# Kernel tuning notes

Measured on AMD Instinct MI355X. Metric: run time of the kernel, lower is better.

The kernel has to match this reference:

```python
import jax, jax.numpy as jnp
import numpy as np

DIM, D_STATE, D_CONV, EXPAND = 512, 16, 4, 2
D_INNER = EXPAND * DIM            # 1024
DT_RANK = (DIM + 15) // 16        # 32
B, L = 2, 2048


def setup_inputs() -> dict:
    key = jax.random.key(0)
    ks = jax.random.split(key, 12)
    s_in = 1.0 / np.sqrt(DIM)
    s_xp = 1.0 / np.sqrt(D_INNER)
    s_dt = 1.0 / np.sqrt(DT_RANK)
    return {
        "x": jax.random.normal(ks[0], (B, L, DIM), jnp.float32),
        "ln_g": jnp.ones((DIM,), jnp.float32),
        "ln_b": jnp.zeros((DIM,), jnp.float32),
        "W_in": jax.random.normal(ks[1], (2 * D_INNER, DIM), jnp.float32) * s_in,
        "conv_w": jax.random.normal(ks[2], (D_INNER, D_CONV), jnp.float32) * 0.5,
        "conv_b": jax.random.normal(ks[3], (D_INNER,), jnp.float32) * 0.1,
        "W_xproj": jax.random.normal(ks[4], (DT_RANK + 2 * D_STATE, D_INNER), jnp.float32) * s_xp,
        "W_dt": jax.random.normal(ks[5], (D_INNER, DT_RANK), jnp.float32) * s_dt,
        "b_dt": jax.random.normal(ks[6], (D_INNER,), jnp.float32) * 0.1 - 4.0,  # softplus -> small dt
        "A_log": jnp.log(jax.random.uniform(ks[7], (D_INNER, D_STATE), jnp.float32, 1.0, 16.0)),
        "Dp": jax.random.normal(ks[8], (D_INNER,), jnp.float32),
        "W_out": jax.random.normal(ks[9], (DIM, D_INNER), jnp.float32) * s_xp,
    }


def _layernorm(x, g, b, eps=1e-5):
    mu = jnp.mean(x, -1, keepdims=True)
    var = jnp.mean(jnp.square(x - mu), -1, keepdims=True)
    return (x - mu) * jax.lax.rsqrt(var + eps) * g + b


def reference(x, ln_g, ln_b, W_in, conv_w, conv_b, W_xproj, W_dt, b_dt, A_log, Dp, W_out):
    h = _layernorm(x, ln_g, ln_b)
    # input projection -> [B,L,2*d_inner]
    xz = jnp.einsum('bld,ed->ble', h, W_in)
    xp, z = jnp.split(xz, 2, axis=-1)
    # depthwise causal conv1d over time (kernel d_conv), then SiLU
    xp_pad = jnp.pad(xp, ((0, 0), (D_CONV - 1, 0), (0, 0)))
    xc = conv_b
    for k in range(D_CONV):
        xc = xc + xp_pad[:, k:k + L, :] * conv_w[:, k]
    xc = jax.nn.silu(xc)
    # x_proj -> dt, B, C
    proj = jnp.einsum('bld,ed->ble', xc, W_xproj)
    dt_r = proj[..., :DT_RANK]
    Bm = proj[..., DT_RANK:DT_RANK + D_STATE]          # [B,L,n]
    Cm = proj[..., DT_RANK + D_STATE:]                 # [B,L,n]
    dt = jax.nn.softplus(jnp.einsum('blr,dr->bld', dt_r, W_dt) + b_dt)  # [B,L,d]
    A = -jnp.exp(A_log)                                # [d,n]
    dA = jnp.exp(jnp.einsum('bld,dn->bldn', dt, A))    # [B,L,d,n]
    dBx = dt[..., None] * Bm[:, :, None, :] * xc[..., None]  # [B,L,d,n]
    # selective scan over time (time-major for lax.scan)
    def step(s, inp):
        dA_t, dBx_t, C_t = inp
        s = s * dA_t + dBx_t                           # [B,d,n]
        y_t = jnp.einsum('bdn,bn->bd', s, C_t)
        return s, y_t
    s0 = jnp.zeros((B, D_INNER, D_STATE), xc.dtype)
    _, ys = jax.lax.scan(step, s0,
                         (jnp.moveaxis(dA, 1, 0), jnp.moveaxis(dBx, 1, 0), jnp.moveaxis(Cm, 1, 0)))
    y = jnp.moveaxis(ys, 0, 1)                         # [B,L,d]
    y = y + xc * Dp
    y = y * jax.nn.silu(z)
    out = jnp.einsum('bld,ed->ble', y, W_out)
    return x + out  # dropout is identity in eval mode
```

## Files before the change

### kernel.cpp

```cpp
#include <hip/hip_runtime.h>
#include <hip/hip_bf16.h>
#include <math.h>

#define B_      2
#define L_      2048
#define DIM_    512
#define DINNER  1024
#define DTRANK  32
#define DSTATE  16
#define DCONV   4
#define BL      (B_ * L_)
#define NCHUNK  64
#define CLEN    (L_ / NCHUNK)

typedef __attribute__((ext_vector_type(8))) short bf16x8;
typedef __attribute__((ext_vector_type(4))) float f32x4;

static __device__ __forceinline__ unsigned short f2bf(float f) {
  __hip_bfloat16 h = __float2bfloat16(f);
  return *(unsigned short*)&h;
}
static __device__ __forceinline__ float bf2f(unsigned short u) {
  return __uint_as_float(((unsigned int)u) << 16);
}

static __device__ __forceinline__ void gload16(const void* g, void* l) {
  __builtin_amdgcn_global_load_lds(
      (const __attribute__((address_space(1))) void*)g,
      (__attribute__((address_space(3))) void*)l, 16, 0, 0);
}

static __device__ __forceinline__ float softplus_f(float acc) {
  return (acc > 20.f) ? acc : __logf(1.f + __expf(acc));
}

__global__ __launch_bounds__(256) void cvt_ln_kernel(
    const float* __restrict__ s0, const float* __restrict__ s1,
    const float* __restrict__ s2, __hip_bfloat16* __restrict__ d0,
    __hip_bfloat16* __restrict__ d1, __hip_bfloat16* __restrict__ d2,
    const float* __restrict__ x, const float* __restrict__ g,
    const float* __restrict__ b, __hip_bfloat16* __restrict__ h) {
  int blk = blockIdx.x;
  if (blk < 1600) {
    int i = (blk * 256 + threadIdx.x) * 4;
    const float* s; __hip_bfloat16* d; int off;
    if (i < 1048576)            { s = s0; d = d0; off = i; }
    else if (i < 1048576+65536) { s = s1; d = d1; off = i - 1048576; }
    else                        { s = s2; d = d2; off = i - 1114112; }
    float4 v = *(const float4*)(s + off);
    d[off + 0] = __float2bfloat16(v.x);
    d[off + 1] = __float2bfloat16(v.y);
    d[off + 2] = __float2bfloat16(v.z);
    d[off + 3] = __float2bfloat16(v.w);
    return;
  }
  int row = (blk - 1600) * 4 + (threadIdx.x >> 6);
  int lane = threadIdx.x & 63;
  const float* xr = x + (size_t)row * DIM_;
  float v[8];
  float sum = 0.f;
#pragma unroll
  for (int i = 0; i < 8; i++) { v[i] = xr[lane + i * 64]; sum += v[i]; }
#pragma unroll
  for (int o = 32; o > 0; o >>= 1) sum += __shfl_xor(sum, o, 64);
  float mu = sum * (1.f / DIM_);
  float vs = 0.f;
#pragma unroll
  for (int i = 0; i < 8; i++) { float dd = v[i] - mu; vs += dd * dd; }
#pragma unroll
  for (int o = 32; o > 0; o >>= 1) vs += __shfl_xor(vs, o, 64);
  float rstd = rsqrtf(vs * (1.f / DIM_) + 1e-5f);
  __hip_bfloat16* hr = h + (size_t)row * DIM_;
#pragma unroll
  for (int i = 0; i < 8; i++) {
    int c = lane + i * 64;
    hr[c] = __float2bfloat16((v[i] - mu) * rstd * g[c] + b[c]);
  }
}

template <bool ADD_RES, bool OUT_BF16>
__global__ __launch_bounds__(256) void gemm_mfma_128(
    const __hip_bfloat16* __restrict__ A, int lda,
    const __hip_bfloat16* __restrict__ Bw, int ldb,
    const float* __restrict__ Res, int ldr,
    void* __restrict__ C, int ldc, int K) {
  __shared__ short As[128 * 64];
  __shared__ short Bs[128 * 64];
  int t = threadIdx.x;
  int n0 = blockIdx.x * 128, m0 = blockIdx.y * 128;
  int w = t >> 6, lane = t & 63;
  int wm = (w >> 1) * 64, wn = (w & 1) * 64;
  int l15 = lane & 15, quad = lane >> 4;
  int lr = lane >> 3, lc = (lane & 7) * 8;
  const short* Ag = (const short*)A + (size_t)(m0 + w * 32 + lr) * lda + lc;
  const short* Bg = (const short*)Bw + (size_t)(n0 + w * 32 + lr) * ldb + lc;
  f32x4 acc[4][4];
#pragma unroll
  for (int i = 0; i < 4; i++)
#pragma unroll
    for (int j = 0; j < 4; j++) acc[i][j] = (f32x4){0.f, 0.f, 0.f, 0.f};
  for (int k0 = 0; k0 < K; k0 += 64) {
    __syncthreads();
#pragma unroll
    for (int p = 0; p < 4; p++) {
      gload16(Ag + (size_t)(p * 8) * lda + k0, &As[(w * 32 + p * 8) * 64]);
      gload16(Bg + (size_t)(p * 8) * ldb + k0, &Bs[(w * 32 + p * 8) * 64]);
    }
    __syncthreads();
#pragma unroll
    for (int kk = 0; kk < 64; kk += 32) {
      bf16x8 af[4], bfr[4];
#pragma unroll
      for (int i = 0; i < 4; i++) {
        af[i] = *(const bf16x8*)&As[(wm + i * 16 + l15) * 64 + kk + quad * 8];
        bfr[i] = *(const bf16x8*)&Bs[(wn + i * 16 + l15) * 64 + kk + quad * 8];
      }
#pragma unroll
      for (int i = 0; i < 4; i++)
#pragma unroll
        for (int j = 0; j < 4; j++)
          acc[i][j] = __builtin_amdgcn_mfma_f32_16x16x32_bf16(
              af[i], bfr[j], acc[i][j], 0, 0, 0);
    }
  }
#pragma unroll
  for (int i = 0; i < 4; i++)
#pragma unroll
    for (int r = 0; r < 4; r++) {
      int row = m0 + wm + i * 16 + quad * 4 + r;
#pragma unroll
      for (int j = 0; j < 4; j++) {
        int col = n0 + wn + j * 16 + l15;
        float v = acc[i][j][r];
        if (ADD_RES) v += Res[(size_t)row * ldr + col];
        if (OUT_BF16)
          ((unsigned short*)C)[(size_t)row * ldc + col] = f2bf(v);
        else
          ((float*)C)[(size_t)row * ldc + col] = v;
      }
    }
}

template <bool ADD_RES>
__global__ __launch_bounds__(256) void gemm_mfma_64(
    const __hip_bfloat16* __restrict__ A, int lda,
    const __hip_bfloat16* __restrict__ Bw, int ldb,
    const float* __restrict__ Res, int ldr,
    float* __restrict__ C, int ldc, int K, size_t czs) {
  __shared__ short As[64 * 64];
  __shared__ short Bs[64 * 64];
  int t = threadIdx.x;
  int n0 = blockIdx.x * 64, m0 = blockIdx.y * 64;
  size_t kbase = (size_t)blockIdx.z * K;
  int w = t >> 6, lane = t & 63;
  int wm = (w >> 1) * 32, wn = (w & 1) * 32;
  int l15 = lane & 15, quad = lane >> 4;
  int lr = lane >> 3, lc = (lane & 7) * 8;
  const short* Ag = (const short*)A + (size_t)(m0 + w * 16 + lr) * lda + lc + kbase;
  const short* Bg = (const short*)Bw + (size_t)(n0 + w * 16 + lr) * ldb + lc + kbase;
  f32x4 acc[2][2];
#pragma unroll
  for (int i = 0; i < 2; i++)
#pragma unroll
    for (int j = 0; j < 2; j++) acc[i][j] = (f32x4){0.f, 0.f, 0.f, 0.f};
  for (int k0 = 0; k0 < K; k0 += 64) {
    __syncthreads();
#pragma unroll
    for (int p = 0; p < 2; p++) {
      gload16(Ag + (size_t)(p * 8) * lda + k0, &As[(w * 16 + p * 8) * 64]);
      gload16(Bg + (size_t)(p * 8) * ldb + k0, &Bs[(w * 16 + p * 8) * 64]);
    }
    __syncthreads();
#pragma unroll
    for (int kk = 0; kk < 64; kk += 32) {
      bf16x8 af[2], bfr[2];
#pragma unroll
      for (int i = 0; i < 2; i++) {
        af[i] = *(const bf16x8*)&As[(wm + i * 16 + l15) * 64 + kk + quad * 8];
        bfr[i] = *(const bf16x8*)&Bs[(wn + i * 16 + l15) * 64 + kk + quad * 8];
      }
#pragma unroll
      for (int i = 0; i < 2; i++)
#pragma unroll
        for (int j = 0; j < 2; j++)
          acc[i][j] = __builtin_amdgcn_mfma_f32_16x16x32_bf16(
              af[i], bfr[j], acc[i][j], 0, 0, 0);
    }
  }
  float* Cz = C + czs * blockIdx.z;
#pragma unroll
  for (int i = 0; i < 2; i++)
#pragma unroll
    for (int r = 0; r < 4; r++) {
      int row = m0 + wm + i * 16 + quad * 4 + r;
#pragma unroll
      for (int j = 0; j < 2; j++) {
        int col = n0 + wn + j * 16 + l15;
        float v = acc[i][j][r];
        if (ADD_RES) v += Res[(size_t)row * ldr + col];
        Cz[(size_t)row * ldc + col] = v;
      }
    }
}

__global__ __launch_bounds__(256) void gemm_proj_conv(
    const unsigned short* __restrict__ xzb,
    const __hip_bfloat16* __restrict__ Bw,
    const float* __restrict__ cw, const float* __restrict__ cb,
    __hip_bfloat16* __restrict__ xc_bf,
    float* __restrict__ C, size_t czs) {
  __shared__ short As[64 * 64];
  __shared__ short Bs[64 * 64];
  __shared__ float cws[256 * 4];
  __shared__ float cbs[256];
  int t = threadIdx.x;
  int m0 = blockIdx.y * 64;
  int kbase = blockIdx.z * 256;
  int w = t >> 6, lane = t & 63;
  int wm = (w >> 1) * 32, wn = (w & 1) * 32;
  int l15 = lane & 15, quad = lane >> 4;
  int lrB = lane >> 3, lcB = (lane & 7) * 8;
  const short* Bg = (const short*)Bw + (size_t)(w * 16 + lrB) * DINNER + lcB + kbase;
  *(float4*)&cws[t * 4] = *(const float4*)(cw + (size_t)(kbase + t) * 4);
  cbs[t] = cb[kbase + t];
  int ar = t >> 2, aq = t & 3;
  int bl = m0 + ar;
  int l = bl & (L_ - 1);
  f32x4 acc[2][2];
#pragma unroll
  for (int i = 0; i < 2; i++)
#pragma unroll
    for (int j = 0; j < 2; j++) acc[i][j] = (f32x4){0.f, 0.f, 0.f, 0.f};
  for (int k0 = 0; k0 < 256; k0 += 64) {
    __syncthreads();
#pragma unroll
    for (int p = 0; p < 2; p++)
      gload16(Bg + k0 + (size_t)(p * 8) * DINNER, &Bs[(w * 16 + p * 8) * 64]);
    int dl0 = k0 + aq * 16;
    const unsigned short* xrow = xzb + (size_t)bl * 2048 + kbase + dl0;
    float o[16];
#pragma unroll
    for (int cc = 0; cc < 16; cc++) o[cc] = cbs[dl0 + cc];
#pragma unroll
    for (int k = 0; k < 4; k++) {
      int off = 3 - k;
      bool ok = (l >= off);
      const unsigned short* src = xrow - (size_t)(ok ? off : 0) * 2048;
      bf16x8 v0 = *(const bf16x8*)(src);
      bf16x8 v1 = *(const bf16x8*)(src + 8);
#pragma unroll
      for (int cc = 0; cc < 8; cc++) {
        float xa = ok ? bf2f((unsigned short)v0[cc]) : 0.f;
        float xb = ok ? bf2f((unsigned short)v1[cc]) : 0.f;
        o[cc]     = fmaf(xa, cws[(dl0 + cc) * 4 + k], o[cc]);
        o[cc + 8] = fmaf(xb, cws[(dl0 + cc + 8) * 4 + k], o[cc + 8]);
      }
    }
    bf16x8 pa, pb;
#pragma unroll
    for (int cc = 0; cc < 8; cc++) {
      float va = o[cc] / (1.f + __expf(-o[cc]));
      float vb = o[cc + 8] / (1.f + __expf(-o[cc + 8]));
      pa[cc] = (short)f2bf(va);
      pb[cc] = (short)f2bf(vb);
    }
    *(bf16x8*)&As[ar * 64 + aq * 16] = pa;
    *(bf16x8*)&As[ar * 64 + aq * 16 + 8] = pb;
    unsigned short* xcd = (unsigned short*)xc_bf + (size_t)bl * DINNER + kbase + dl0;
    *(bf16x8*)xcd = pa;
    *(bf16x8*)(xcd + 8) = pb;
    __syncthreads();
#pragma unroll
    for (int kk = 0; kk < 64; kk += 32) {
      bf16x8 af[2], bfr[2];
#pragma unroll
      for (int i = 0; i < 2; i++) {
        af[i] = *(const bf16x8*)&As[(wm + i * 16 + l15) * 64 + kk + quad * 8];
        bfr[i] = *(const bf16x8*)&Bs[(wn + i * 16 + l15) * 64 + kk + quad * 8];
      }
#pragma unroll
      for (int i = 0; i < 2; i++)
#pragma unroll
        for (int j = 0; j < 2; j++)
          acc[i][j] = __builtin_amdgcn_mfma_f32_16x16x32_bf16(
              af[i], bfr[j], acc[i][j], 0, 0, 0);
    }
  }
  float* Cz = C + czs * blockIdx.z;
#pragma unroll
  for (int i = 0; i < 2; i++)
#pragma unroll
    for (int r = 0; r < 4; r++) {
      int row = m0 + wm + i * 16 + quad * 4 + r;
#pragma unroll
      for (int j = 0; j < 2; j++) {
        int col = wn + j * 16 + l15;
        Cz[(size_t)row * 64 + col] = acc[i][j][r];
      }
    }
}

__global__ __launch_bounds__(256) void dt_kernel(
    const float* __restrict__ pp, float* __restrict__ proj,
    const float* __restrict__ Wdt, const float* __restrict__ bdt,
    float* __restrict__ dt) {
  int blk = blockIdx.x;
  int dgrp = blk & 3;
  int bl0 = (blk >> 2) * 8;
  int tid = threadIdx.x;
  int d = dgrp * 256 + tid;
  __shared__ float pr[8 * 64];
  float w[32];
#pragma unroll
  for (int q = 0; q < 8; q++) {
    float4 wv = *(const float4*)(Wdt + (size_t)d * 32 + q * 4);
    w[q * 4 + 0] = wv.x; w[q * 4 + 1] = wv.y;
    w[q * 4 + 2] = wv.z; w[q * 4 + 3] = wv.w;
  }
  float bias = bdt[d];
  if (tid < 128) {
    int o4 = bl0 * 16 + tid;
    float4 v0 = ((const float4*)pp)[o4];
    float4 v1 = ((const float4*)pp)[o4 + 65536];
    float4 v2 = ((const float4*)pp)[o4 + 131072];
    float4 v3 = ((const float4*)pp)[o4 + 196608];
    float4 s;
    s.x = (v0.x + v1.x) + (v2.x + v3.x);
    s.y = (v0.y + v1.y) + (v2.y + v3.y);
    s.z = (v0.z + v1.z) + (v2.z + v3.z);
    s.w = (v0.w + v1.w) + (v2.w + v3.w);
    ((float4*)pr)[tid] = s;
    if (dgrp == 0) *(float4*)(proj + (size_t)bl0 * 64 + tid * 4) = s;
  }
  __syncthreads();
#pragma unroll
  for (int row = 0; row < 8; row++) {
    float a0 = 0.f, a1 = 0.f, a2 = 0.f, a3 = 0.f;
#pragma unroll
    for (int q = 0; q < 8; q++) {
      float4 pv = *(const float4*)&pr[row * 64 + q * 4];
      a0 = fmaf(pv.x, w[q * 4 + 0], a0);
      a1 = fmaf(pv.y, w[q * 4 + 1], a1);
      a2 = fmaf(pv.z, w[q * 4 + 2], a2);
      a3 = fmaf(pv.w, w[q * 4 + 3], a3);
    }
    float acc = bias + ((a0 + a1) + (a2 + a3));
    dt[(size_t)(bl0 + row) * DINNER + d] = softplus_f(acc);
  }
}

__global__ __launch_bounds__(256) void scan1_kernel(
    const float* __restrict__ dt, const __hip_bfloat16* __restrict__ xc_bf,
    const float* __restrict__ proj, const float* __restrict__ A_log,
    float* __restrict__ T, float* __restrict__ E) {
  int bid = blockIdx.x;
  int dgrp4 = bid & 15;
  int c = (bid >> 4) & (NCHUNK - 1);
  int b = bid >> 10;
  int tid = threadIdx.x;
  int dl = tid >> 2;
  int n4 = tid & 3;
  int d0 = dgrp4 * 64;
  int d = d0 + dl;
  int l0 = c * CLEN;
  __shared__ float dts[CLEN * 64];
  __shared__ float xcs[CLEN * 64];
  __shared__ float Bsh[CLEN * 16];
  for (int i = tid; i < CLEN * 16; i += 256) {
    int row = i >> 4, c4 = i & 15;
    *(float4*)&dts[row * 64 + c4 * 4] =
        *(const float4*)(dt + (size_t)(b * L_ + l0 + row) * DINNER + d0 + c4 * 4);
  }
  {
    int row = tid >> 3, c8 = tid & 7;
    bf16x8 v = *(const bf16x8*)((const unsigned short*)xc_bf +
                                (size_t)(b * L_ + l0 + row) * DINNER + d0 + c8 * 8);
#pragma unroll
    for (int k = 0; k < 8; k++)
      xcs[row * 64 + c8 * 8 + k] = bf2f((unsigned short)v[k]);
  }
  if (tid < CLEN * 4) {
    int row = tid >> 2, c4 = tid & 3;
    *(float4*)&Bsh[row * 16 + c4 * 4] =
        *(const float4*)(proj + (size_t)(b * L_ + l0 + row) * 64 + 32 + c4 * 4);
  }
  float4 av = *(const float4*)(A_log + (size_t)d * 16 + n4 * 4);
  float Aa[4] = {-__expf(av.x), -__expf(av.y), -__expf(av.z), -__expf(av.w)};
  __syncthreads();
  float Tn[4] = {1.f, 1.f, 1.f, 1.f};
  float En[4] = {0.f, 0.f, 0.f, 0.f};
#pragma unroll 8
  for (int l = 0; l < CLEN; l++) {
    float dtv = dts[l * 64 + dl];
    float dx = dtv * xcs[l * 64 + dl];
#pragma unroll
    for (int j = 0; j < 4; j++) {
      float dA = __expf(dtv * Aa[j]);
      Tn[j] *= dA;
      En[j] = En[j] * dA + dx * Bsh[l * 16 + n4 * 4 + j];
    }
  }
  size_t o = (((size_t)b * NCHUNK + c) * DINNER + d) * 16 + n4 * 4;
  *(float4*)&T[o] = *(float4*)Tn;
  *(float4*)&E[o] = *(float4*)En;
}

__global__ __launch_bounds__(256) void combine_kernel(
    float* __restrict__ T, const float* __restrict__ E) {
  int idx = blockIdx.x * 256 + threadIdx.x;
  int b = idx >> 14;
  int dn = idx & 16383;
  size_t base = (size_t)b * NCHUNK * (DINNER * 16) + dn;
  float s = 0.f;
#pragma unroll
  for (int batch = 0; batch < 4; batch++) {
    float t[16], e[16];
#pragma unroll
    for (int j = 0; j < 16; j++) {
      size_t o = base + (size_t)(batch * 16 + j) * (DINNER * 16);
      t[j] = T[o]; e[j] = E[o];
    }
#pragma unroll
    for (int j = 0; j < 16; j++) {
      T[base + (size_t)(batch * 16 + j) * (DINNER * 16)] = s;
      s = t[j] * s + e[j];
    }
  }
}

__global__ __launch_bounds__(256) void scan2_kernel(
    const float* __restrict__ dt, const __hip_bfloat16* __restrict__ xc_bf,
    const float* __restrict__ proj, const float* __restrict__ A_log,
    const float* __restrict__ Sstart, const float* __restrict__ Dp,
    unsigned short* __restrict__ xzb) {
  int bid = blockIdx.x;
  int dgrp = bid & 3;
  int c = (bid >> 2) & (NCHUNK - 1);
  int b = bid >> 8;
  int tid = threadIdx.x;
  int d = dgrp * 256 + tid;
  int l0 = c * CLEN;
  __shared__ float Bsh[CLEN * 16];
  __shared__ float Csh[CLEN * 16];
  for (int i = tid; i < CLEN * 16; i += 256) {
    int row = i >> 4, nn = i & 15;
    const float* pr = proj + (size_t)(b * L_ + l0 + row) * 64;
    Bsh[i] = pr[32 + nn];
    Csh[i] = pr[48 + nn];
  }
  float dtr[CLEN], xvr[CLEN];
  unsigned short zr[CLEN];
#pragma unroll
  for (int l = 0; l < CLEN; l++) {
    size_t bl = (size_t)(b * L_ + l0 + l);
    dtr[l] = dt[bl * DINNER + d];
    xvr[l] = __bfloat162float(xc_bf[bl * DINNER + d]);
    zr[l] = xzb[bl * 2048 + 1024 + d];
  }
  float Aa[16], s[16];
  size_t sb = (((size_t)b * NCHUNK + c) * DINNER + d) * 16;
#pragma unroll
  for (int q = 0; q < 4; q++) {
    float4 av = *(const float4*)(A_log + (size_t)d * 16 + q * 4);
    Aa[q * 4 + 0] = -__expf(av.x); Aa[q * 4 + 1] = -__expf(av.y);
    Aa[q * 4 + 2] = -__expf(av.z); Aa[q * 4 + 3] = -__expf(av.w);
    float4 sv = *(const float4*)(Sstart + sb + q * 4);
    s[q * 4 + 0] = sv.x; s[q * 4 + 1] = sv.y;
    s[q * 4 + 2] = sv.z; s[q * 4 + 3] = sv.w;
  }
  float Dv = Dp[d];
  __syncthreads();
#pragma unroll
  for (int l = 0; l < CLEN; l++) {
    float dtv = dtr[l];
    float xv = xvr[l];
    float dx = dtv * xv;
    float y = 0.f;
#pragma unroll
    for (int n = 0; n < 16; n++) {
      float dA = __expf(dtv * Aa[n]);
      s[n] = s[n] * dA + dx * Bsh[l * 16 + n];
      y += s[n] * Csh[l * 16 + n];
    }
    float zv = bf2f(zr[l]);
    float gate = zv / (1.f + __expf(-zv));
    xzb[(size_t)(b * L_ + l0 + l) * 2048 + d] = f2bf((y + xv * Dv) * gate);
  }
}

extern "C" void kernel_launch(void* const* d_in, const int* in_sizes, int n_in,
                              void* d_out, int out_size, void* d_ws, size_t ws_size,
                              hipStream_t stream) {
  const float* x      = (const float*)d_in[0];
  const float* ln_g   = (const float*)d_in[1];
  const float* ln_b   = (const float*)d_in[2];
  const float* W_in   = (const float*)d_in[3];
  const float* conv_w = (const float*)d_in[4];
  const float* conv_b = (const float*)d_in[5];
  const float* W_xprj = (const float*)d_in[6];
  const float* W_dt   = (const float*)d_in[7];
  const float* b_dt   = (const float*)d_in[8];
  const float* A_log  = (const float*)d_in[9];
  const float* Dp     = (const float*)d_in[10];
  const float* W_out  = (const float*)d_in[11];
  float* out = (float*)d_out;

  float* ws     = (float*)d_ws;
  float* xzb_f  = ws;
  float* xcbf_f = xzb_f + 4194304;
  float* proj   = xcbf_f + 2097152;
  float* pp     = proj + 262144;
  float* dtb    = pp + 1048576;
  float* T      = dtb + 4194304;
  float* E      = T + 2097152;
  float* hbf_f  = E + 2097152;
  float* wbf    = hbf_f + 1048576;

  unsigned short* xzb   = (unsigned short*)xzb_f;
  __hip_bfloat16* xc_bf = (__hip_bfloat16*)xcbf_f;
  __hip_bfloat16* h_bf  = (__hip_bfloat16*)hbf_f;
  __hip_bfloat16* Wb_in = (__hip_bfloat16*)wbf;
  __hip_bfloat16* Wb_xp = Wb_in + 1048576;
  __hip_bfloat16* Wb_out = Wb_xp + 65536;
  __hip_bfloat16* y_bf  = (__hip_bfloat16*)xzb;

  cvt_ln_kernel<<<1600 + BL / 4, 256, 0, stream>>>(
      W_in, W_xprj, W_out, Wb_in, Wb_xp, Wb_out, x, ln_g, ln_b, h_bf);
  gemm_mfma_128<false, true><<<dim3(2 * DINNER / 128, BL / 128), 256, 0, stream>>>(
      h_bf, DIM_, Wb_in, DIM_, nullptr, 0, xzb, 2 * DINNER, DIM_);
  gemm_proj_conv<<<dim3(1, BL / 64, 4), 256, 0, stream>>>(
      xzb, Wb_xp, conv_w, conv_b, xc_bf, pp, 262144);
  dt_kernel<<<(BL / 8) * 4, 256, 0, stream>>>(pp, proj, W_dt, b_dt, dtb);
  scan1_kernel<<<B_ * NCHUNK * 16, 256, 0, stream>>>(dtb, xc_bf, proj, A_log, T, E);
  combine_kernel<<<(B_ * DINNER * 16) / 256, 256, 0, stream>>>(T, E);
  scan2_kernel<<<B_ * NCHUNK * 4, 256, 0, stream>>>(dtb, xc_bf, proj, A_log, T, Dp, xzb);
  gemm_mfma_64<true><<<dim3(DIM_ / 64, BL / 64, 1), 256, 0, stream>>>(
      y_bf, 2048, Wb_out, DINNER, x, DIM_, out, DIM_, DINNER, 0);
}
```

Measured before the change: 191.9 us.

## Split scan2 state dimension across 4 lanes and stage inputs in LDS

The second-pass chunked scan kernel now gives each channel to four threads, each holding four of the sixteen state elements, and combines the partial outputs with lane shuffles. Grid size grows fourfold (16 channel groups of 64 instead of 4 of 256). dt, xc and z tiles are loaded cooperatively into shared memory with vectorized loads instead of each thread holding per-timestep register arrays. The aim is more parallelism, lower register pressure and coalesced loads, at the cost of more blocks, a shuffle reduction, and a store done by only a quarter of the lanes.

New measurement: 240.5 us. 1.25x slower.

```diff
diff --git a/kernel.cpp b/kernel.cpp
--- a/kernel.cpp
+++ b/kernel.cpp
@@ -434,57 +434,74 @@
     const float* __restrict__ Sstart, const float* __restrict__ Dp,
     unsigned short* __restrict__ xzb) {
   int bid = blockIdx.x;
-  int dgrp = bid & 3;
-  int c = (bid >> 2) & (NCHUNK - 1);
-  int b = bid >> 8;
+  int dgrp = bid & 15;
+  int c = (bid >> 4) & (NCHUNK - 1);
+  int b = bid >> 10;
   int tid = threadIdx.x;
-  int d = dgrp * 256 + tid;
+  int dl = tid >> 2;
+  int n4 = tid & 3;
+  int d0 = dgrp * 64;
+  int d = d0 + dl;
   int l0 = c * CLEN;
+  __shared__ float dts[CLEN * 64];
+  __shared__ float xcs[CLEN * 64];
+  __shared__ unsigned short zs[CLEN * 64];
   __shared__ float Bsh[CLEN * 16];
   __shared__ float Csh[CLEN * 16];
   for (int i = tid; i < CLEN * 16; i += 256) {
-    int row = i >> 4, nn = i & 15;
-    const float* pr = proj + (size_t)(b * L_ + l0 + row) * 64;
-    Bsh[i] = pr[32 + nn];
-    Csh[i] = pr[48 + nn];
-  }
-  float dtr[CLEN], xvr[CLEN];
-  unsigned short zr[CLEN];
-#pragma unroll
-  for (int l = 0; l < CLEN; l++) {
-    size_t bl = (size_t)(b * L_ + l0 + l);
-    dtr[l] = dt[bl * DINNER + d];
-    xvr[l] = __bfloat162float(xc_bf[bl * DINNER + d]);
-    zr[l] = xzb[bl * 2048 + 1024 + d];
-  }
-  float Aa[16], s[16];
-  size_t sb = (((size_t)b * NCHUNK + c) * DINNER + d) * 16;
-#pragma unroll
-  for (int q = 0; q < 4; q++) {
-    float4 av = *(const float4*)(A_log + (size_t)d * 16 + q * 4);
-    Aa[q * 4 + 0] = -__expf(av.x); Aa[q * 4 + 1] = -__expf(av.y);
-    Aa[q * 4 + 2] = -__expf(av.z); Aa[q * 4 + 3] = -__expf(av.w);
-    float4 sv = *(const float4*)(Sstart + sb + q * 4);
-    s[q * 4 + 0] = sv.x; s[q * 4 + 1] = sv.y;
-    s[q * 4 + 2] = sv.z; s[q * 4 + 3] = sv.w;
-  }
+    int row = i >> 4, c4 = i & 15;
+    *(float4*)&dts[row * 64 + c4 * 4] =
+        *(const float4*)(dt + (size_t)(b * L_ + l0 + row) * DINNER + d0 + c4 * 4);
+  }
+  {
+    int row = tid >> 3, c8 = tid & 7;
+    bf16x8 v = *(const bf16x8*)((const unsigned short*)xc_bf +
+                                (size_t)(b * L_ + l0 + row) * DINNER + d0 + c8 * 8);
+#pragma unroll
+    for (int k = 0; k < 8; k++)
+      xcs[row * 64 + c8 * 8 + k] = bf2f((unsigned short)v[k]);
+    bf16x8 zv = *(const bf16x8*)(xzb + (size_t)(b * L_ + l0 + row) * 2048 +
+                                 1024 + d0 + c8 * 8);
+    *(bf16x8*)&zs[row * 64 + c8 * 8] = zv;
+  }
+  {
+    int row = tid >> 3, q = tid & 7;
+    float4 v = *(const float4*)(proj + (size_t)(b * L_ + l0 + row) * 64 + 32 + q * 4);
+    if (q < 4) *(float4*)&Bsh[row * 16 + q * 4] = v;
+    else       *(float4*)&Csh[row * 16 + (q - 4) * 4] = v;
+  }
+  float4 av = *(const float4*)(A_log + (size_t)d * 16 + n4 * 4);
+  float Aa[4] = {-__expf(av.x), -__expf(av.y), -__expf(av.z), -__expf(av.w)};
+  size_t sb = (((size_t)b * NCHUNK + c) * DINNER + d) * 16 + n4 * 4;
+  float4 sv = *(const float4*)(Sstart + sb);
+  float s[4] = {sv.x, sv.y, sv.z, sv.w};
   float Dv = Dp[d];
   __syncthreads();
+  float yr[CLEN];
 #pragma unroll
   for (int l = 0; l < CLEN; l++) {
-    float dtv = dtr[l];
-    float xv = xvr[l];
-    float dx = dtv * xv;
+    float dtv = dts[l * 64 + dl];
+    float dx = dtv * xcs[l * 64 + dl];
     float y = 0.f;
 #pragma unroll
-    for (int n = 0; n < 16; n++) {
-      float dA = __expf(dtv * Aa[n]);
-      s[n] = s[n] * dA + dx * Bsh[l * 16 + n];
-      y += s[n] * Csh[l * 16 + n];
-    }
-    float zv = bf2f(zr[l]);
-    float gate = zv / (1.f + __expf(-zv));
-    xzb[(size_t)(b * L_ + l0 + l) * 2048 + d] = f2bf((y + xv * Dv) * gate);
+    for (int j = 0; j < 4; j++) {
+      float dA = __expf(dtv * Aa[j]);
+      s[j] = s[j] * dA + dx * Bsh[l * 16 + n4 * 4 + j];
+      y += s[j] * Csh[l * 16 + n4 * 4 + j];
+    }
+    yr[l] = y;
+  }
+#pragma unroll
+  for (int l = 0; l < CLEN; l++) {
+    float y = yr[l];
+    y += __shfl_xor(y, 1, 64);
+    y += __shfl_xor(y, 2, 64);
+    if (n4 == 0) {
+      float xv = xcs[l * 64 + dl];
+      float zv = bf2f(zs[l * 64 + dl]);
+      float gate = zv / (1.f + __expf(-zv));
+      xzb[(size_t)(b * L_ + l0 + l) * 2048 + d] = f2bf((y + xv * Dv) * gate);
+    }
   }
 }
 
@@ -533,7 +550,7 @@
   dt_kernel<<<(BL / 8) * 4, 256, 0, stream>>>(pp, proj, W_dt, b_dt, dtb);
   scan1_kernel<<<B_ * NCHUNK * 16, 256, 0, stream>>>(dtb, xc_bf, proj, A_log, T, E);
   combine_kernel<<<(B_ * DINNER * 16) / 256, 256, 0, stream>>>(T, E);
-  scan2_kernel<<<B_ * NCHUNK * 4, 256, 0, stream>>>(dtb, xc_bf, proj, A_log, T, Dp, xzb);
+  scan2_kernel<<<B_ * NCHUNK * 16, 256, 0, stream>>>(dtb, xc_bf, proj, A_log, T, Dp, xzb);
   gemm_mfma_64<true><<<dim3(DIM_ / 64, BL / 64, 1), 256, 0, stream>>>(
       y_bf, 2048, Wb_out, DINNER, x, DIM_, out, DIM_, DINNER, 0);
 }
```
